# Performance work log

Measured on AMD Instinct MI355X. Metric: run time of the kernel, lower is better.

The kernel has to match this reference:

```python
import jax, jax.numpy as jnp
import numpy as np

B, N, DIM_IN, DIM_INNER, DIM_OUT, WINDOW = 4, 4096, 1024, 1024, 1024, 128


def setup_inputs() -> dict:
    key = jax.random.key(0)
    k1, k2, k3, k4 = jax.random.split(key, 4)
    x = jax.random.normal(k1, (B, N, DIM_IN), dtype=jnp.float32)
    # to_qkv: Linear(dim_in, 3*dim_inner, bias=False); stored as [in, 3*inner] for x @ W
    w_qkv = jax.random.normal(k2, (DIM_IN, 3 * DIM_INNER), dtype=jnp.float32) / np.sqrt(DIM_IN)
    # to_out: Linear(dim_inner, dim_out) with bias
    w_out = jax.random.normal(k3, (DIM_INNER, DIM_OUT), dtype=jnp.float32) / np.sqrt(DIM_INNER)
    b_out = jax.random.normal(k4, (DIM_OUT,), dtype=jnp.float32) * 0.01
    return {"x": x, "w_qkv": w_qkv, "w_out": w_out, "b_out": b_out}


def reference(x, w_qkv, w_out, b_out):
    b, n, _ = x.shape
    w = WINDOW
    scale = DIM_INNER ** (-0.5)
    # n is a multiple of window, so pad_to_multiple is a no-op
    qkv = jnp.einsum('bnd,de->bne', x, w_qkv)
    q, k, v = jnp.split(qkv, 3, axis=-1)
    nw = n // w
    win = lambda t: t.reshape(b, nw, w, DIM_INNER)  # b (w n) d -> b w n d
    q, k, v = win(q), win(k), win(v)
    # pad one zero block at the front of the window axis
    kp = jnp.pad(k, ((0, 0), (1, 0), (0, 0), (0, 0)))
    # concat previous block + current block along token axis -> (b, nw, 2w, d)
    k2 = jnp.concatenate([kp[:, :-1], kp[:, 1:]], axis=2)
    # NOTE: faithful to source bug: the lambda references k (not t), so v is
    # overwritten with the concatenated k blocks as well.
    v2 = k2
    sim = jnp.einsum('bwid,bwjd->bwij', q, k2) * scale  # (b, nw, w, 2w)
    i, j = w, 2 * w
    mask = jnp.triu(jnp.ones((i, j), dtype=bool), j - i + 1)  # causal within lookback window
    mask_value = -jnp.finfo(sim.dtype).max
    sim = jnp.where(mask[None, None], mask_value, sim)
    attn = jax.nn.softmax(sim, axis=-1)
    out = jnp.einsum('bwij,bwjd->bwid', attn, v2)
    out = out.reshape(b, n, DIM_INNER)[:, :n]
    return jnp.einsum('bnd,de->bne', out, w_out) + b_out
```

## Files before the change

### kernel.cpp

```cpp
#include <hip/hip_runtime.h>
#include <float.h>


#define B_SZ 4
#define SEQ 4096
#define DIM 1024
#define WIN 128
#define NWIN 32
#define TW 256
#define NROWS (B_SZ * SEQ)
#define KPAD 4224

typedef float f32x4 __attribute__((ext_vector_type(4)));
typedef __bf16 bf16x8 __attribute__((ext_vector_type(8)));
typedef unsigned short u16x8 __attribute__((ext_vector_type(8)));

__device__ __forceinline__ unsigned short f2b(float f) {
    unsigned int u = __float_as_uint(f);
    u += 0x7FFF + ((u >> 16) & 1);
    return (unsigned short)(u >> 16);
}

__device__ __forceinline__ void gld_lds16(const unsigned short* g, unsigned short* l) {
    __builtin_amdgcn_global_load_lds(
        (const __attribute__((address_space(1))) void*)g,
        (__attribute__((address_space(3))) void*)l, 16, 0, 0);
}

__device__ __forceinline__ bf16x8 lds_read_swz(const unsigned short* tb, int row, int kbyte) {
    int L = row * 128 + kbyte;
    L ^= ((L >> 9) & 1) << 5;
    return *(const bf16x8*)((const char*)tb + L);
}

#define BAR __builtin_amdgcn_s_barrier()
#define PRI1 __builtin_amdgcn_s_setprio(1)
#define PRI0 __builtin_amdgcn_s_setprio(0)
#define LGKM0 do { asm volatile("s_waitcnt lgkmcnt(0)" ::: "memory"); \
                   __builtin_amdgcn_sched_barrier(0); } while (0)
#define VMW(N) do { asm volatile("s_waitcnt vmcnt(" #N ")" ::: "memory"); \
                    __builtin_amdgcn_sched_barrier(0); } while (0)

#define LDAF(BUF, MH)                                                        \
    _Pragma("unroll") for (int m_ = 0; m_ < 4; ++m_)                         \
    _Pragma("unroll") for (int ks_ = 0; ks_ < 2; ++ks_)                      \
        afq[MH][m_][ks_] = lds_read_swz(bufA[BUF],                           \
            wr * 128 + (MH) * 64 + m_ * 16 + fr, ks_ * 64 + kby);

#define LDBF(BUF, NH)                                                        \
    _Pragma("unroll") for (int n_ = 0; n_ < 2; ++n_)                         \
    _Pragma("unroll") for (int ks_ = 0; ks_ < 2; ++ks_)                      \
        bfq[n_][ks_] = lds_read_swz(bufB[BUF],                               \
            wc * 64 + (NH) * 32 + n_ * 16 + fr, ks_ * 64 + kby);

#define MFQ(MH, NH)                                                          \
    _Pragma("unroll") for (int ks_ = 0; ks_ < 2; ++ks_)                      \
    _Pragma("unroll") for (int m_ = 0; m_ < 4; ++m_)                         \
    _Pragma("unroll") for (int n_ = 0; n_ < 2; ++n_)                         \
        acc[(MH) * 4 + m_][(NH) * 2 + n_] =                                  \
            __builtin_amdgcn_mfma_f32_16x16x32_bf16(afq[MH][m_][ks_],        \
                bfq[n_][ks_], acc[(MH) * 4 + m_][(NH) * 2 + n_], 0, 0, 0);

#define STG_HA(BUF, HALF, K0)                                                \
    { gld_lds16(A + soffA[(HALF) * 2 + 0] + (K0), bufA[BUF] + ldst[(HALF) * 2 + 0]); \
      gld_lds16(A + soffA[(HALF) * 2 + 1] + (K0), bufA[BUF] + ldst[(HALF) * 2 + 1]); }
#define STG_HB(BUF, HALF, K0)                                                \
    { gld_lds16(Bt + soffB[(HALF) * 2 + 0] + (K0), bufB[BUF] + ldst[(HALF) * 2 + 0]); \
      gld_lds16(Bt + soffB[(HALF) * 2 + 1] + (K0), bufB[BUF] + ldst[(HALF) * 2 + 1]); }

__device__ __forceinline__ void core256(
    const unsigned short* __restrict__ A, int lda,
    const unsigned short* __restrict__ Bt, int ldb, int K,
    unsigned short* lds, f32x4 (&acc)[8][4],
    int wid, int lane, int wr, int wc)
{
    unsigned short* bufA[2] = { lds, lds + 32768 };
    unsigned short* bufB[2] = { lds + 16384, lds + 49152 };

    const int kby = (lane >> 4) * 16;
    const int fr = lane & 15;

    int soffA[4], soffB[4], ldst[4];
#pragma unroll
    for (int hj = 0; hj < 4; ++hj) {
        const int half = hj >> 1, j = hj & 1;
        const int P = half * 16384 + wid * 2048 + j * 1024 + lane * 16;
        const int L = P ^ (((P >> 9) & 1) << 5);
        const int row = L >> 7, col = (L & 127) >> 1;
        soffA[hj] = row * lda + col;
        soffB[hj] = row * ldb + col;
        ldst[hj] = (half * 16384 + wid * 2048 + j * 1024) >> 1;
    }

    bf16x8 afq[2][4][2], bfq[2][2];
#pragma unroll
    for (int m = 0; m < 8; ++m)
#pragma unroll
        for (int n = 0; n < 4; ++n) acc[m][n] = (f32x4){0.f, 0.f, 0.f, 0.f};

    STG_HA(0, 0, 0); STG_HA(0, 1, 0); STG_HB(0, 0, 0); STG_HB(0, 1, 0);
    STG_HA(1, 0, 64); STG_HA(1, 1, 64); STG_HB(1, 0, 64);
    VMW(6);
    BAR;

    const int NITER = K >> 7;
#pragma unroll 1
    for (int i = 0; i < NITER; ++i) {
        const bool st = (i + 1 < NITER);
        const int ku1 = (2 * i + 1) * 64;
        const int ku2 = (2 * i + 2) * 64;
        const int ku3 = (2 * i + 3) * 64;

        LDAF(0, 0); LDBF(0, 0);
        STG_HB(1, 1, ku1);
        BAR; LGKM0; PRI1; MFQ(0, 0); PRI0; BAR;
        LDAF(0, 1);
        BAR; LGKM0; PRI1; MFQ(1, 0); PRI0; BAR;
        LDBF(0, 1);
        if (st) STG_HA(0, 0, ku2);
        BAR; LGKM0; PRI1; MFQ(1, 1); PRI0; BAR;
        if (st) { STG_HA(0, 1, ku2); VMW(4); } else { VMW(0); }
        BAR; PRI1; MFQ(0, 1); PRI0; BAR;
        LDAF(1, 0); LDBF(1, 0);
        if (st) STG_HB(0, 0, ku2);
        BAR; LGKM0; PRI1; MFQ(0, 0); PRI0; BAR;
        LDAF(1, 1);
        if (st) STG_HB(0, 1, ku2);
        BAR; LGKM0; PRI1; MFQ(1, 0); PRI0; BAR;
        LDBF(1, 1);
        if (st) STG_HA(1, 0, ku3);
        BAR; LGKM0; PRI1; MFQ(1, 1); PRI0; BAR;
        if (st) { STG_HA(1, 1, ku3); STG_HB(1, 0, ku3); VMW(6); } else { VMW(0); }
        BAR; PRI1; MFQ(0, 1); PRI0; BAR;
    }
}

__global__ __launch_bounds__(256) void k_prep_x(const float* __restrict__ x,
                                                unsigned short* __restrict__ xb)
{
    int i = blockIdx.x * 256 + threadIdx.x;
    float4 a = *(const float4*)&x[(size_t)i * 8];
    float4 b = *(const float4*)&x[(size_t)i * 8 + 4];
    ushort4 lo, hi;
    lo.x = f2b(a.x); lo.y = f2b(a.y); lo.z = f2b(a.z); lo.w = f2b(a.w);
    hi.x = f2b(b.x); hi.y = f2b(b.y); hi.z = f2b(b.z); hi.w = f2b(b.w);
    *(ushort4*)&xb[(size_t)i * 8] = lo;
    *(ushort4*)&xb[(size_t)i * 8 + 4] = hi;
}

__global__ __launch_bounds__(256) void k_transpose(const float* __restrict__ src,
    int src_ld, int col0, int R, unsigned short* __restrict__ dst)
{
    __shared__ float T[32][33];
    const int r0 = blockIdx.y * 32, c0 = blockIdx.x * 32;
    const int cx = threadIdx.x & 31, ry = threadIdx.x >> 5;
#pragma unroll
    for (int i = 0; i < 4; ++i)
        T[ry + 8 * i][cx] = src[(size_t)(r0 + ry + 8 * i) * src_ld + col0 + c0 + cx];
    __syncthreads();
#pragma unroll
    for (int i = 0; i < 4; ++i)
        dst[(size_t)(c0 + ry + 8 * i) * R + r0 + cx] = f2b(T[cx][ry + 8 * i]);
}

__global__ __launch_bounds__(256) void k_zero_kpad(unsigned short* __restrict__ kbuf)
{
    int t = blockIdx.x * 256 + threadIdx.x;
    int b = t >> 14, r = t & 16383;
    float4 z = {0.f, 0.f, 0.f, 0.f};
    *(float4*)&kbuf[(size_t)b * KPAD * DIM + (size_t)r * 8] = z;
}

__global__ __launch_bounds__(512, 2) void k_gemm_qk(
    const unsigned short* __restrict__ xb, const unsigned short* __restrict__ wqkvT,
    unsigned short* __restrict__ qbuf, unsigned short* __restrict__ kbuf)
{
    __shared__ unsigned short lds[65536];
    const int tid = threadIdx.x, wid = tid >> 6, lane = tid & 63;
    const int wr = wid >> 2, wc = wid & 3;
    const int wg = blockIdx.x;
    const int x = (wg & 7) * 64 + (wg >> 3);
    const int bm = (x & 63) * 256;
    const int bn = (x >> 6) * 256;

    f32x4 acc[8][4];
    core256(xb + (size_t)bm * DIM, DIM, wqkvT + (size_t)bn * DIM, DIM, DIM,
            lds, acc, wid, lane, wr, wc);

    const int fr = lane & 15;
#pragma unroll
    for (int m = 0; m < 8; ++m) {
        const int row0 = bm + wr * 128 + m * 16 + (lane >> 4) * 4;
#pragma unroll
        for (int n = 0; n < 4; ++n) {
            const int col = bn + wc * 64 + n * 16 + fr;
            if (col < DIM) {
#pragma unroll
                for (int r = 0; r < 4; ++r)
                    qbuf[(size_t)(row0 + r) * DIM + col] = f2b(acc[m][n][r]);
            } else {
                const int d = col - DIM;
                const int b = row0 >> 12, tok0 = row0 & 4095;
#pragma unroll
                for (int r = 0; r < 4; ++r)
                    kbuf[((size_t)b * KPAD + 128 + tok0 + r) * DIM + d] = f2b(acc[m][n][r]);
            }
        }
    }
}

__global__ __launch_bounds__(512, 2) void k_out(
    const unsigned short* __restrict__ aout, const unsigned short* __restrict__ woutT,
    const float* __restrict__ bias, float* __restrict__ out)
{
    __shared__ unsigned short lds[65536];
    const int tid = threadIdx.x, wid = tid >> 6, lane = tid & 63;
    const int wr = wid >> 2, wc = wid & 3;
    const int wg = blockIdx.x;
    const int x = (wg & 7) * 32 + (wg >> 3);
    const int bm = (x & 63) * 256;
    const int bn = (x >> 6) * 256;

    f32x4 acc[8][4];
    core256(aout + (size_t)bm * DIM, DIM, woutT + (size_t)bn * DIM, DIM, DIM,
            lds, acc, wid, lane, wr, wc);

    const int fr = lane & 15;
#pragma unroll
    for (int m = 0; m < 8; ++m) {
        const int row0 = bm + wr * 128 + m * 16 + (lane >> 4) * 4;
#pragma unroll
        for (int n = 0; n < 4; ++n) {
            const int col = bn + wc * 64 + n * 16 + fr;
            const float bb = bias[col];
#pragma unroll
            for (int r = 0; r < 4; ++r)
                out[(size_t)(row0 + r) * DIM + col] = acc[m][n][r] + bb;
        }
    }
}

__global__ __launch_bounds__(512) void k_simsm(
    const unsigned short* __restrict__ qbuf, const unsigned short* __restrict__ kbuf,
    unsigned short* __restrict__ attnb)
{
    __shared__ unsigned short As[64 * 64];
    __shared__ unsigned short Bs[256 * 64];
    __shared__ float smax[4][64];
    __shared__ float ssum[4][64];

    const int mh = blockIdx.x, win = blockIdx.y;
    const int b = win >> 5, w = win & 31;
    const int tid = threadIdx.x, wid = tid >> 6, lane = tid & 63;
    const int wr = wid >> 2, wc = wid & 3;
    const int hi = lane >> 4, fr = lane & 15;

    const unsigned short* A  = qbuf + (size_t)(b * SEQ + w * WIN + mh * 64) * DIM;
    const unsigned short* Bt = kbuf + ((size_t)b * KPAD + w * WIN) * DIM;

    f32x4 acc[2][4];
#pragma unroll
    for (int m = 0; m < 2; ++m)
#pragma unroll
        for (int n = 0; n < 4; ++n) acc[m][n] = (f32x4){0.f, 0.f, 0.f, 0.f};

    for (int k0 = 0; k0 < DIM; k0 += 64) {
        gld_lds16(A + (size_t)(wid * 8 + (lane >> 3)) * DIM + k0 + (lane & 7) * 8,
                  As + wid * 512);
#pragma unroll
        for (int it = 0; it < 4; ++it)
            gld_lds16(Bt + (size_t)(it * 64 + wid * 8 + (lane >> 3)) * DIM + k0 + (lane & 7) * 8,
                      Bs + it * 4096 + wid * 512);
        __syncthreads();
#pragma unroll
        for (int ks = 0; ks < 2; ++ks) {
            bf16x8 af[2], bf[4];
            const int kof = ks * 32 + hi * 8;
#pragma unroll
            for (int m = 0; m < 2; ++m)
                af[m] = *(const bf16x8*)(As + (wr * 32 + m * 16 + fr) * 64 + kof);
#pragma unroll
            for (int n = 0; n < 4; ++n)
                bf[n] = *(const bf16x8*)(Bs + (wc * 64 + n * 16 + fr) * 64 + kof);
#pragma unroll
            for (int m = 0; m < 2; ++m)
#pragma unroll
                for (int n = 0; n < 4; ++n)
                    acc[m][n] = __builtin_amdgcn_mfma_f32_16x16x32_bf16(
                        af[m], bf[n], acc[m][n], 0, 0, 0);
        }
        __syncthreads();
    }

    const float scale = 0.03125f;
    float ms[2][4][4];
#pragma unroll
    for (int m = 0; m < 2; ++m)
#pragma unroll
        for (int r = 0; r < 4; ++r) {
            const int qi = mh * 64 + wr * 32 + m * 16 + hi * 4 + r;
#pragma unroll
            for (int n = 0; n < 4; ++n) {
                const int jc = wc * 64 + n * 16 + fr;
                ms[m][n][r] = (jc > qi + WIN) ? -FLT_MAX : acc[m][n][r] * scale;
            }
        }

    float pmv[2][4];
#pragma unroll
    for (int m = 0; m < 2; ++m)
#pragma unroll
        for (int r = 0; r < 4; ++r) {
            float pm = fmaxf(fmaxf(ms[m][0][r], ms[m][1][r]),
                             fmaxf(ms[m][2][r], ms[m][3][r]));
#pragma unroll
            for (int off = 1; off < 16; off <<= 1) pm = fmaxf(pm, __shfl_xor(pm, off));
            pmv[m][r] = pm;
        }
    if (fr == 0) {
#pragma unroll
        for (int m = 0; m < 2; ++m)
#pragma unroll
            for (int r = 0; r < 4; ++r)
                smax[wc][wr * 32 + m * 16 + hi * 4 + r] = pmv[m][r];
    }
    __syncthreads();

    float e[2][4][4], psv[2][4];
#pragma unroll
    for (int m = 0; m < 2; ++m)
#pragma unroll
        for (int r = 0; r < 4; ++r) {
            const int rl = wr * 32 + m * 16 + hi * 4 + r;
            const float rm = fmaxf(fmaxf(smax[0][rl], smax[1][rl]),
                                   fmaxf(smax[2][rl], smax[3][rl]));
            float s = 0.f;
#pragma unroll
            for (int n = 0; n < 4; ++n) {
                e[m][n][r] = expf(ms[m][n][r] - rm);
                s += e[m][n][r];
            }
#pragma unroll
            for (int off = 1; off < 16; off <<= 1) s += __shfl_xor(s, off);
            psv[m][r] = s;
        }
    if (fr == 0) {
#pragma unroll
        for (int m = 0; m < 2; ++m)
#pragma unroll
            for (int r = 0; r < 4; ++r)
                ssum[wc][wr * 32 + m * 16 + hi * 4 + r] = psv[m][r];
    }
    __syncthreads();

#pragma unroll
    for (int m = 0; m < 2; ++m)
#pragma unroll
        for (int r = 0; r < 4; ++r) {
            const int rl = wr * 32 + m * 16 + hi * 4 + r;
            const float inv = 1.f / (ssum[0][rl] + ssum[1][rl] + ssum[2][rl] + ssum[3][rl]);
            const size_t rowg = (size_t)win * WIN + mh * 64 + rl;
#pragma unroll
            for (int n = 0; n < 4; ++n)
                attnb[rowg * TW + wc * 64 + n * 16 + fr] = f2b(e[m][n][r] * inv);
        }
}

__global__ __launch_bounds__(256) void k_pv(
    const unsigned short* __restrict__ attnb, const unsigned short* __restrict__ kbuf,
    unsigned short* __restrict__ aout)
{
    __shared__ unsigned short As[128 * 64];
    __shared__ unsigned short Bs[128 * 64];

    const int win = blockIdx.y, ct = blockIdx.x;
    const int b = win >> 5, w = win & 31;
    const int tid = threadIdx.x, wv = tid >> 6, lane = tid & 63;
    const int wr = wv >> 1, wc = wv & 1;

    const unsigned short* Ap = attnb + (size_t)win * WIN * TW;
    const unsigned short* Kp = kbuf + ((size_t)b * KPAD + w * WIN) * DIM + ct * 128;

    f32x4 acc[4][4];
#pragma unroll
    for (int m = 0; m < 4; ++m)
#pragma unroll
        for (int n = 0; n < 4; ++n) acc[m][n] = (f32x4){0.f, 0.f, 0.f, 0.f};

    for (int k0 = 0; k0 < TW; k0 += 64) {
        u16x8 v[4];
#pragma unroll
        for (int it = 0; it < 4; ++it)
            v[it] = *(const u16x8*)&Kp[(size_t)(k0 + it * 16 + (tid >> 4)) * DIM + (tid & 15) * 8];
        __syncthreads();
#pragma unroll
        for (int it = 0; it < 4; ++it) {
            const int tok = it * 16 + (tid >> 4);
            const int d0 = (tid & 15) * 8;
#pragma unroll
            for (int ee = 0; ee < 8; ++ee)
                Bs[(d0 + ee) * 64 + tok] = v[it][ee];
        }
#pragma unroll
        for (int it = 0; it < 4; ++it)
            gld_lds16(Ap + (size_t)(wv * 32 + it * 8 + (lane >> 3)) * TW + k0 + (lane & 7) * 8,
                      As + (wv * 32 + it * 8) * 64);
        __syncthreads();

#pragma unroll
        for (int ks = 0; ks < 2; ++ks) {
            bf16x8 af[4], bfr[4];
            const int kof = ks * 32 + (lane >> 4) * 8;
#pragma unroll
            for (int m = 0; m < 4; ++m)
                af[m] = *(const bf16x8*)(As + (wr * 64 + m * 16 + (lane & 15)) * 64 + kof);
#pragma unroll
            for (int n = 0; n < 4; ++n)
                bfr[n] = *(const bf16x8*)(Bs + (wc * 64 + n * 16 + (lane & 15)) * 64 + kof);
#pragma unroll
            for (int m = 0; m < 4; ++m)
#pragma unroll
                for (int n = 0; n < 4; ++n)
                    acc[m][n] = __builtin_amdgcn_mfma_f32_16x16x32_bf16(
                        af[m], bfr[n], acc[m][n], 0, 0, 0);
        }
        __syncthreads();
    }

#pragma unroll
    for (int m = 0; m < 4; ++m) {
        const int row0 = wr * 64 + m * 16 + (lane >> 4) * 4;
#pragma unroll
        for (int n = 0; n < 4; ++n) {
            const int col = ct * 128 + wc * 64 + n * 16 + (lane & 15);
#pragma unroll
            for (int r = 0; r < 4; ++r)
                aout[((size_t)b * SEQ + w * WIN + row0 + r) * DIM + col] =
                    f2b(acc[m][n][r]);
        }
    }
}

extern "C" void kernel_launch(void* const* d_in, const int* in_sizes, int n_in,
                              void* d_out, int out_size, void* d_ws, size_t ws_size,
                              hipStream_t stream)
{
    const float* x     = (const float*)d_in[0];
    const float* w_qkv = (const float*)d_in[1];
    const float* w_out = (const float*)d_in[2];
    const float* b_out = (const float*)d_in[3];
    float* out = (float*)d_out;

    char* p = (char*)d_ws;
    unsigned short* xb    = (unsigned short*)p; p += (size_t)NROWS * DIM * 2;
    unsigned short* wqkvT = (unsigned short*)p; p += (size_t)2 * DIM * DIM * 2;
    unsigned short* woutT = (unsigned short*)p; p += (size_t)DIM * DIM * 2;
    unsigned short* qbuf  = (unsigned short*)p; p += (size_t)NROWS * DIM * 2;
    unsigned short* kbuf  = (unsigned short*)p; p += (size_t)B_SZ * KPAD * DIM * 2;
    unsigned short* attnb = (unsigned short*)p; p += (size_t)NROWS * TW * 2;
    unsigned short* aout  = (unsigned short*)p; p += (size_t)NROWS * DIM * 2;

    k_prep_x<<<NROWS * DIM / 8 / 256, 256, 0, stream>>>(x, xb);
    k_transpose<<<dim3(2 * DIM / 32, DIM / 32), 256, 0, stream>>>(w_qkv, 3 * DIM, 0, DIM, wqkvT);
    k_transpose<<<dim3(DIM / 32, DIM / 32), 256, 0, stream>>>(w_out, DIM, 0, DIM, woutT);
    k_zero_kpad<<<256, 256, 0, stream>>>(kbuf);

    k_gemm_qk<<<512, 512, 0, stream>>>(xb, wqkvT, qbuf, kbuf);
    k_simsm<<<dim3(2, B_SZ * NWIN), 512, 0, stream>>>(qbuf, kbuf, attnb);
    k_pv<<<dim3(DIM / 128, B_SZ * NWIN), 256, 0, stream>>>(attnb, kbuf, aout);
    k_out<<<256, 512, 0, stream>>>(aout, woutT, b_out, out);
}
```

Before: 367.7 us.

## Fuse similarity-softmax and PV kernels, keep probabilities in LDS with XOR swizzle

Merges the score/softmax kernel and the attention-times-V kernel into one kernel. The bf16 probability tile stays in shared memory, so the attention matrix is no longer written to and read back from global memory, and one launch is removed. LDS tiles are XOR-swizzled to reduce bank conflicts. In exchange the grid for the PV stage drops from 1024 blocks to 256 blocks of 512 threads, each looping serially over 8 column tiles with a large ~74KB LDS footprint, which lowers parallelism and occupancy.

```diff
diff --git a/kernel.cpp b/kernel.cpp
--- a/kernel.cpp
+++ b/kernel.cpp
@@ -240,14 +240,17 @@
     }
 }
 
-__global__ __launch_bounds__(512) void k_simsm(
+__global__ __launch_bounds__(512) void k_attn(
     const unsigned short* __restrict__ qbuf, const unsigned short* __restrict__ kbuf,
-    unsigned short* __restrict__ attnb)
-{
-    __shared__ unsigned short As[64 * 64];
-    __shared__ unsigned short Bs[256 * 64];
-    __shared__ float smax[4][64];
-    __shared__ float ssum[4][64];
+    unsigned short* __restrict__ aout)
+{
+    __shared__ __align__(16) char smem[75776];
+    unsigned short* As  = (unsigned short*)smem;
+    unsigned short* Bs  = (unsigned short*)(smem + 8192);
+    char*           Bs2 = smem;
+    char*           Ps  = smem + 40960;
+    float*          smax = (float*)(smem + 73728);
+    float*          ssum = (float*)(smem + 74752);
 
     const int mh = blockIdx.x, win = blockIdx.y;
     const int b = win >> 5, w = win & 31;
@@ -255,8 +258,12 @@
     const int wr = wid >> 2, wc = wid & 3;
     const int hi = lane >> 4, fr = lane & 15;
 
-    const unsigned short* A  = qbuf + (size_t)(b * SEQ + w * WIN + mh * 64) * DIM;
-    const unsigned short* Bt = kbuf + ((size_t)b * KPAD + w * WIN) * DIM;
+    const unsigned short* Aq = qbuf + (size_t)(b * SEQ + w * WIN + mh * 64) * DIM;
+    const unsigned short* Kp = kbuf + ((size_t)b * KPAD + w * WIN) * DIM;
+
+    const int arow = wid * 8 + (lane >> 3);
+    const int acs  = ((lane & 7) ^ (arow & 7)) * 8;
+    const int adst = arow * 64 + (lane & 7) * 8;
 
     f32x4 acc[2][4];
 #pragma unroll
@@ -265,23 +272,26 @@
         for (int n = 0; n < 4; ++n) acc[m][n] = (f32x4){0.f, 0.f, 0.f, 0.f};
 
     for (int k0 = 0; k0 < DIM; k0 += 64) {
-        gld_lds16(A + (size_t)(wid * 8 + (lane >> 3)) * DIM + k0 + (lane & 7) * 8,
-                  As + wid * 512);
+        gld_lds16(Aq + (size_t)arow * DIM + k0 + acs, As + adst);
 #pragma unroll
         for (int it = 0; it < 4; ++it)
-            gld_lds16(Bt + (size_t)(it * 64 + wid * 8 + (lane >> 3)) * DIM + k0 + (lane & 7) * 8,
-                      Bs + it * 4096 + wid * 512);
+            gld_lds16(Kp + (size_t)(it * 64 + arow) * DIM + k0 + acs,
+                      Bs + it * 4096 + adst);
         __syncthreads();
 #pragma unroll
         for (int ks = 0; ks < 2; ++ks) {
+            const int kb = ks * 64 + hi * 16;
             bf16x8 af[2], bf[4];
-            const int kof = ks * 32 + hi * 8;
-#pragma unroll
-            for (int m = 0; m < 2; ++m)
-                af[m] = *(const bf16x8*)(As + (wr * 32 + m * 16 + fr) * 64 + kof);
-#pragma unroll
-            for (int n = 0; n < 4; ++n)
-                bf[n] = *(const bf16x8*)(Bs + (wc * 64 + n * 16 + fr) * 64 + kof);
+#pragma unroll
+            for (int m = 0; m < 2; ++m) {
+                const int P = (wr * 32 + m * 16 + fr) * 128 + kb;
+                af[m] = *(const bf16x8*)((char*)As + (P ^ (((P >> 7) & 7) << 4)));
+            }
+#pragma unroll
+            for (int n = 0; n < 4; ++n) {
+                const int P = (wc * 64 + n * 16 + fr) * 128 + kb;
+                bf[n] = *(const bf16x8*)((char*)Bs + (P ^ (((P >> 7) & 7) << 4)));
+            }
 #pragma unroll
             for (int m = 0; m < 2; ++m)
 #pragma unroll
@@ -322,7 +332,7 @@
         for (int m = 0; m < 2; ++m)
 #pragma unroll
             for (int r = 0; r < 4; ++r)
-                smax[wc][wr * 32 + m * 16 + hi * 4 + r] = pmv[m][r];
+                smax[wc * 64 + wr * 32 + m * 16 + hi * 4 + r] = pmv[m][r];
     }
     __syncthreads();
 
@@ -332,8 +342,8 @@
 #pragma unroll
         for (int r = 0; r < 4; ++r) {
             const int rl = wr * 32 + m * 16 + hi * 4 + r;
-            const float rm = fmaxf(fmaxf(smax[0][rl], smax[1][rl]),
-                                   fmaxf(smax[2][rl], smax[3][rl]));
+            const float rm = fmaxf(fmaxf(smax[rl], smax[64 + rl]),
+                                   fmaxf(smax[128 + rl], smax[192 + rl]));
             float s = 0.f;
 #pragma unroll
             for (int n = 0; n < 4; ++n) {
@@ -349,7 +359,7 @@
         for (int m = 0; m < 2; ++m)
 #pragma unroll
             for (int r = 0; r < 4; ++r)
-                ssum[wc][wr * 32 + m * 16 + hi * 4 + r] = psv[m][r];
+                ssum[wc * 64 + wr * 32 + m * 16 + hi * 4 + r] = psv[m][r];
     }
     __syncthreads();
 
@@ -358,85 +368,74 @@
 #pragma unroll
         for (int r = 0; r < 4; ++r) {
             const int rl = wr * 32 + m * 16 + hi * 4 + r;
-            const float inv = 1.f / (ssum[0][rl] + ssum[1][rl] + ssum[2][rl] + ssum[3][rl]);
-            const size_t rowg = (size_t)win * WIN + mh * 64 + rl;
-#pragma unroll
-            for (int n = 0; n < 4; ++n)
-                attnb[rowg * TW + wc * 64 + n * 16 + fr] = f2b(e[m][n][r] * inv);
-        }
-}
-
-__global__ __launch_bounds__(256) void k_pv(
-    const unsigned short* __restrict__ attnb, const unsigned short* __restrict__ kbuf,
-    unsigned short* __restrict__ aout)
-{
-    __shared__ unsigned short As[128 * 64];
-    __shared__ unsigned short Bs[128 * 64];
-
-    const int win = blockIdx.y, ct = blockIdx.x;
-    const int b = win >> 5, w = win & 31;
-    const int tid = threadIdx.x, wv = tid >> 6, lane = tid & 63;
-    const int wr = wv >> 1, wc = wv & 1;
-
-    const unsigned short* Ap = attnb + (size_t)win * WIN * TW;
-    const unsigned short* Kp = kbuf + ((size_t)b * KPAD + w * WIN) * DIM + ct * 128;
-
-    f32x4 acc[4][4];
-#pragma unroll
-    for (int m = 0; m < 4; ++m)
-#pragma unroll
-        for (int n = 0; n < 4; ++n) acc[m][n] = (f32x4){0.f, 0.f, 0.f, 0.f};
-
-    for (int k0 = 0; k0 < TW; k0 += 64) {
-        u16x8 v[4];
-#pragma unroll
-        for (int it = 0; it < 4; ++it)
-            v[it] = *(const u16x8*)&Kp[(size_t)(k0 + it * 16 + (tid >> 4)) * DIM + (tid & 15) * 8];
-        __syncthreads();
-#pragma unroll
-        for (int it = 0; it < 4; ++it) {
-            const int tok = it * 16 + (tid >> 4);
-            const int d0 = (tid & 15) * 8;
-#pragma unroll
-            for (int ee = 0; ee < 8; ++ee)
-                Bs[(d0 + ee) * 64 + tok] = v[it][ee];
-        }
-#pragma unroll
-        for (int it = 0; it < 4; ++it)
-            gld_lds16(Ap + (size_t)(wv * 32 + it * 8 + (lane >> 3)) * TW + k0 + (lane & 7) * 8,
-                      As + (wv * 32 + it * 8) * 64);
-        __syncthreads();
-
-#pragma unroll
-        for (int ks = 0; ks < 2; ++ks) {
-            bf16x8 af[4], bfr[4];
-            const int kof = ks * 32 + (lane >> 4) * 8;
-#pragma unroll
-            for (int m = 0; m < 4; ++m)
-                af[m] = *(const bf16x8*)(As + (wr * 64 + m * 16 + (lane & 15)) * 64 + kof);
-#pragma unroll
-            for (int n = 0; n < 4; ++n)
-                bfr[n] = *(const bf16x8*)(Bs + (wc * 64 + n * 16 + (lane & 15)) * 64 + kof);
-#pragma unroll
-            for (int m = 0; m < 4; ++m)
-#pragma unroll
-                for (int n = 0; n < 4; ++n)
-                    acc[m][n] = __builtin_amdgcn_mfma_f32_16x16x32_bf16(
-                        af[m], bfr[n], acc[m][n], 0, 0, 0);
-        }
-        __syncthreads();
-    }
-
-#pragma unroll
-    for (int m = 0; m < 4; ++m) {
-        const int row0 = wr * 64 + m * 16 + (lane >> 4) * 4;
-#pragma unroll
-        for (int n = 0; n < 4; ++n) {
-            const int col = ct * 128 + wc * 64 + n * 16 + (lane & 15);
-#pragma unroll
-            for (int r = 0; r < 4; ++r)
-                aout[((size_t)b * SEQ + w * WIN + row0 + r) * DIM + col] =
-                    f2b(acc[m][n][r]);
+            const float inv =
+                1.f / (ssum[rl] + ssum[64 + rl] + ssum[128 + rl] + ssum[192 + rl]);
+#pragma unroll
+            for (int n = 0; n < 4; ++n) {
+                const int jc = wc * 64 + n * 16 + fr;
+                const int P = rl * 512 + jc * 2;
+                *(unsigned short*)(Ps + (P ^ (((P >> 9) & 7) << 4))) =
+                    f2b(e[m][n][r] * inv);
+            }
+        }
+    __syncthreads();
+
+    const size_t orow0 = (size_t)(b * SEQ + w * WIN + mh * 64);
+#pragma unroll 1
+    for (int dt = 0; dt < 8; ++dt) {
+        f32x4 acc2[2][2];
+#pragma unroll
+        for (int m = 0; m < 2; ++m)
+#pragma unroll
+            for (int n = 0; n < 2; ++n) acc2[m][n] = (f32x4){0.f, 0.f, 0.f, 0.f};
+
+#pragma unroll 1
+        for (int ts = 0; ts < 4; ++ts) {
+#pragma unroll
+            for (int i = 0; i < 2; ++i) {
+                const int tok = i * 32 + (tid >> 4);
+                const int d0 = (tid & 15) * 8;
+                u16x8 v = *(const u16x8*)&Kp[(size_t)(ts * 64 + tok) * DIM + dt * 128 + d0];
+#pragma unroll
+                for (int ee = 0; ee < 8; ++ee) {
+                    const int P = (d0 + ee) * 128 + tok * 2;
+                    *(unsigned short*)(Bs2 + (P ^ ((((P >> 7) ^ (P >> 10)) & 7) << 4))) = v[ee];
+                }
+            }
+            __syncthreads();
+#pragma unroll
+            for (int ks = 0; ks < 2; ++ks) {
+                bf16x8 pa[2], kb2[2];
+                const int tb = ts * 128 + ks * 64 + hi * 16;
+#pragma unroll
+                for (int m = 0; m < 2; ++m) {
+                    const int P = (wr * 32 + m * 16 + fr) * 512 + tb;
+                    pa[m] = *(const bf16x8*)(Ps + (P ^ (((P >> 9) & 7) << 4)));
+                }
+#pragma unroll
+                for (int n = 0; n < 2; ++n) {
+                    const int P = (wc * 32 + n * 16 + fr) * 128 + ks * 64 + hi * 16;
+                    kb2[n] = *(const bf16x8*)(Bs2 + (P ^ ((((P >> 7) ^ (P >> 10)) & 7) << 4)));
+                }
+#pragma unroll
+                for (int m = 0; m < 2; ++m)
+#pragma unroll
+                    for (int n = 0; n < 2; ++n)
+                        acc2[m][n] = __builtin_amdgcn_mfma_f32_16x16x32_bf16(
+                            pa[m], kb2[n], acc2[m][n], 0, 0, 0);
+            }
+            __syncthreads();
+        }
+#pragma unroll
+        for (int m = 0; m < 2; ++m) {
+            const int row0 = wr * 32 + m * 16 + hi * 4;
+#pragma unroll
+            for (int n = 0; n < 2; ++n) {
+                const int col = dt * 128 + wc * 32 + n * 16 + fr;
+#pragma unroll
+                for (int r = 0; r < 4; ++r)
+                    aout[(orow0 + row0 + r) * DIM + col] = f2b(acc2[m][n][r]);
+            }
         }
     }
 }
@@ -457,7 +456,6 @@
     unsigned short* woutT = (unsigned short*)p; p += (size_t)DIM * DIM * 2;
     unsigned short* qbuf  = (unsigned short*)p; p += (size_t)NROWS * DIM * 2;
     unsigned short* kbuf  = (unsigned short*)p; p += (size_t)B_SZ * KPAD * DIM * 2;
-    unsigned short* attnb = (unsigned short*)p; p += (size_t)NROWS * TW * 2;
     unsigned short* aout  = (unsigned short*)p; p += (size_t)NROWS * DIM * 2;
 
     k_prep_x<<<NROWS * DIM / 8 / 256, 256, 0, stream>>>(x, xb);
@@ -466,7 +464,6 @@
     k_zero_kpad<<<256, 256, 0, stream>>>(kbuf);
 
     k_gemm_qk<<<512, 512, 0, stream>>>(xb, wqkvT, qbuf, kbuf);
-    k_simsm<<<dim3(2, B_SZ * NWIN), 512, 0, stream>>>(qbuf, kbuf, attnb);
-    k_pv<<<dim3(DIM / 128, B_SZ * NWIN), 256, 0, stream>>>(attnb, kbuf, aout);
+    k_attn<<<dim3(2, B_SZ * NWIN), 512, 0, stream>>>(qbuf, kbuf, aout);
     k_out<<<256, 512, 0, stream>>>(aout, woutT, b_out, out);
 }
```

Measured after the change: 347.9 us. -5.4%, faster.
